# Performance work log

Measured on AMD Instinct MI355X. Metric: run time of the kernel, lower is better.

Reference implementation:

```python
import jax, jax.numpy as jnp
import numpy as np

N_NODES = 100000
N_EDGES = 1200000
K1, K2 = 4096, 256  # TopKPooling ratios (int ratio => absolute k in PyG)
NEG_SLOPE = 0.01    # nn.LeakyReLU default


def leaky(v):
    return jnp.where(v >= 0, v, NEG_SLOPE * v)


def gcn_conv(x, src, dst, w, W, b):
    """PyG GCNConv: x @ W, symmetric-normalized aggregation with self-loops, + bias.
    Removed edges are represented by weight 0 (identical math to edge removal)."""
    N = x.shape[0]
    x = x @ W                                            # [N, out]
    deg = jax.ops.segment_sum(w, dst, num_segments=N) + 1.0  # +1 self-loop
    dinv = jax.lax.rsqrt(deg)
    norm = dinv[src] * w * dinv[dst]                     # per-edge norm
    agg = jax.ops.segment_sum(x[src] * norm[:, None], dst, num_segments=N)
    agg = agg + x * (dinv * dinv)[:, None]               # self-loop term
    return agg + b


def topk_pool(x, src, dst, w, p, k):
    """PyG TopKPooling: score = tanh(x.p/||p||), keep top-k, scale by score,
    relabel edges; dropped edges get weight 0 (mapped to node 0 harmlessly)."""
    N = x.shape[0]
    score = jnp.tanh((x @ p) / jnp.linalg.norm(p))
    top_scores, perm = jax.lax.top_k(score, k)
    x_new = x[perm] * top_scores[:, None]
    mapping = jnp.zeros(N, jnp.int32).at[perm].set(jnp.arange(k, dtype=jnp.int32))
    kept = jnp.zeros(N, dtype=bool).at[perm].set(True)
    valid = kept[src] & kept[dst]
    return x_new, mapping[src], mapping[dst], jnp.where(valid, w, 0.0)


def setup_inputs() -> dict:
    key = jax.random.key(0)
    ks = jax.random.split(key, 12)
    pos = jax.random.normal(ks[0], (N_NODES, 3), dtype=jnp.float32)
    edge_index = jax.random.randint(ks[1], (2, N_EDGES), 0, N_NODES, dtype=jnp.int64)

    def glorot(k, shape):
        lim = np.sqrt(6.0 / (shape[0] + shape[-1]))
        return jax.random.uniform(k, shape, jnp.float32, -lim, lim)

    return {
        "pos": pos,
        "edge_index": edge_index,
        "W1": glorot(ks[2], (3, 64)),    "b1": jnp.zeros((64,), jnp.float32),
        "W2": glorot(ks[3], (64, 128)),  "b2": jnp.zeros((128,), jnp.float32),
        "W3": glorot(ks[4], (128, 256)), "b3": jnp.zeros((256,), jnp.float32),
        "p1": jax.random.normal(ks[5], (64,), jnp.float32),
        "p2": jax.random.normal(ks[6], (256,), jnp.float32),
        "fcW": glorot(ks[7], (256 * 256, 512)),
        "fcb": jnp.zeros((512,), jnp.float32),
    }


def reference(pos, edge_index, W1, b1, W2, b2, W3, b3, p1, p2, fcW, fcb):
    src, dst = edge_index[0], edge_index[1]
    w = jnp.ones(src.shape[0], dtype=pos.dtype)

    x = leaky(gcn_conv(pos, src, dst, w, W1, b1))          # [N, 64]
    x, src, dst, w = topk_pool(x, src, dst, w, p1, K1)     # [4096, 64]
    x = leaky(gcn_conv(x, src, dst, w, W2, b2))            # [4096, 128]
    x = leaky(gcn_conv(x, src, dst, w, W3, b3))            # [4096, 256]
    x, src, dst, w = topk_pool(x, src, dst, w, p2, K2)     # [256, 256]

    x = x.T.reshape(-1)                                    # transpose(0,1) + flatten
    return x @ fcW + fcb                                   # [512]
```

## Files before the change

kernel.cpp:

```cpp
#include <hip/hip_runtime.h>
#include <cstdint>
#include <cstddef>

#define NNODES 100000
#define NEDGES 1200000
#define KP1 4096
#define KP2 256
#define CAP_CAND 16384
#define CAP1 48
#define CAP2 48
#define NSAMP 2048
#define TAURANK 167
#define NXCD 8
#define DRANGE 12500

typedef unsigned long long u64;
typedef unsigned int u32;

__device__ __forceinline__ double leakyd(double v){ return v >= 0.0 ? v : 0.01*v; }

__device__ __forceinline__ u64 mono64(double d){
  u64 b = (u64)__double_as_longlong(d);
  return (b & 0x8000000000000000ull) ? ~b : (b | 0x8000000000000000ull);
}

__device__ __forceinline__ void get_edge(const int* eb, int flag, int e, int& s, int& d){
  if (flag){ s = eb[2*e]; d = eb[2*(NEDGES+e)]; }
  else     { s = eb[e];   d = eb[NEDGES+e]; }
}

__global__ __launch_bounds__(256) void k_zero(int* cnt1, int* mapping, int* rank1, int* rank2, int* cnt){
  int n = blockIdx.x*256 + threadIdx.x;
  if (n < NNODES){ cnt1[n] = 0; mapping[n] = -1; }
  if (n < CAP_CAND) rank1[n] = 0;
  if (n < KP1) rank2[n] = 0;
  if (n < 64) cnt[n] = 0;
}

__global__ void k_meta(const int* eb, const float* p1, const float* p2, int* meta, double* dscal){
  __shared__ double red[256];
  int t = threadIdx.x;
  double s1 = 0.0;
  if (t < 64){ double v = (double)p1[t]; s1 = v*v; }
  red[t] = s1; __syncthreads();
  for (int w = 128; w > 0; w >>= 1){ if (t < w) red[t] += red[t+w]; __syncthreads(); }
  if (t == 0) dscal[0] = 1.0 / sqrt(red[0]);
  __syncthreads();
  double v2 = (double)p2[t];
  red[t] = v2*v2; __syncthreads();
  for (int w = 128; w > 0; w >>= 1){ if (t < w) red[t] += red[t+w]; __syncthreads(); }
  if (t == 0){
    dscal[1] = 1.0 / sqrt(red[0]);
    int is64 = 1;
    for (int i = 1; i <= 127; i += 2) if (eb[i] != 0){ is64 = 0; break; }
    meta[0] = is64;
  }
}

__global__ __launch_bounds__(256) void k_scatter(const int* eb, const int* meta, int* cnt1, int* csrf){
  int e = (blockIdx.x >> 3)*256 + threadIdx.x;
  int x = blockIdx.x & 7;
  if (e >= NEDGES) return;
  int s, d; get_edge(eb, meta[0], e, s, d);
  if (d/DRANGE != x) return;
  int slot = atomicAdd(&cnt1[d], 1);
  if (slot < CAP1) csrf[(size_t)d*CAP1 + slot] = s;
}

__global__ void k_prep(const int* cnt1, const float* pos, double4* posw){
  int n = blockIdx.x*256 + threadIdx.x;
  if (n >= NNODES) return;
  double di = 1.0 / sqrt((double)cnt1[n] + 1.0);
  double4 v;
  v.x = (double)pos[3*n+0]*di;
  v.y = (double)pos[3*n+1]*di;
  v.z = (double)pos[3*n+2]*di;
  v.w = di;
  posw[n] = v;
}

__global__ __launch_bounds__(256) void k_score1(const int* cnt1, const int* csrf,
                         const double4* posw,
                         const float* W1, const float* b1, const float* p1,
                         double* score1raw, u64* key1){
  int gid = blockIdx.x*256 + threadIdx.x;
  int n = gid >> 2;
  int l = gid & 3;
  if (n >= NNODES) return;
  int c = cnt1[n]; if (c > CAP1) c = CAP1;
  const int4* row = (const int4*)(csrf + (size_t)n*CAP1);
  int4 r0 = row[l];
  int4 r1 = make_int4(0,0,0,0);
  int4 r2 = make_int4(0,0,0,0);
  if (c > 16) r1 = row[l+4];
  if (c > 32) r2 = row[l+8];
  double t0 = 0.0, t1 = 0.0, t2 = 0.0;
  auto g = [&](int sidx, bool liv){
    if (liv){
      double4 p = posw[sidx];
      t0 += p.x; t1 += p.y; t2 += p.z;
    }
  };
  int j0 = l*4;
  g(r0.x, j0+0 < c); g(r0.y, j0+1 < c); g(r0.z, j0+2 < c); g(r0.w, j0+3 < c);
  int j1 = l*4 + 16;
  g(r1.x, j1+0 < c); g(r1.y, j1+1 < c); g(r1.z, j1+2 < c); g(r1.w, j1+3 < c);
  int j2 = l*4 + 32;
  g(r2.x, j2+0 < c); g(r2.y, j2+1 < c); g(r2.z, j2+2 < c); g(r2.w, j2+3 < c);
  for (int o = 1; o < 4; o <<= 1){
    t0 += __shfl_xor(t0, o, 64);
    t1 += __shfl_xor(t1, o, 64);
    t2 += __shfl_xor(t2, o, 64);
  }
  double4 pwn = posw[n];
  double di = pwn.w;
  t0 = (t0 + pwn.x)*di;
  t1 = (t1 + pwn.y)*di;
  t2 = (t2 + pwn.z)*di;
  double acc = 0.0;
  #pragma unroll
  for (int f16 = 0; f16 < 16; ++f16){
    int f = l*16 + f16;
    double h = t0*(double)W1[f] + t1*(double)W1[64+f] + t2*(double)W1[128+f] + (double)b1[f];
    acc += leakyd(h) * (double)p1[f];
  }
  acc += __shfl_xor(acc, 1, 64);
  acc += __shfl_xor(acc, 2, 64);
  if (l == 0){
    score1raw[n] = acc;
    key1[n] = (mono64(acc) & ~0x1FFFFull) | (u64)(131071 - n);
  }
}

__global__ __launch_bounds__(256) void k_tau(const u64* key1, u64* tau){
  __shared__ u64 smp[NSAMP];
  int t = threadIdx.x;
  int sid = blockIdx.x*256 + t;
  for (int i = t; i < NSAMP; i += 256) smp[i] = key1[(size_t)i*48];
  __syncthreads();
  u64 mykey = smp[sid];
  int rank = 0;
  for (int j = 0; j < NSAMP; ++j) rank += (smp[j] > mykey) ? 1 : 0;
  if (rank == TAURANK) tau[0] = mykey;
}

__global__ void k_collect(const u64* key1, const u64* tau, int* cand, u64* candkey, int* cnt){
  int n = blockIdx.x*256 + threadIdx.x;
  if (n >= NNODES) return;
  u64 k = key1[n];
  if (k >= tau[0]){
    int p = atomicAdd(&cnt[0], 1);
    if (p < CAP_CAND){ cand[p] = n; candkey[p] = k; }
  }
}

__global__ __launch_bounds__(256) void k_rankA(const u64* candkey, const int* cnt, int* rank){
  int C = cnt[0]; if (C > CAP_CAND) C = CAP_CAND;
  int ci = blockIdx.x, kj = blockIdx.y;
  if (ci*256 >= C || kj*256 >= C) return;
  __shared__ u64 tile[256];
  int t = threadIdx.x;
  int kidx = kj*256 + t;
  tile[t] = (kidx < C) ? candkey[kidx] : 0ull;
  __syncthreads();
  int idx = ci*256 + t;
  if (idx >= C) return;
  u64 mykey = candkey[idx];
  int r = 0;
  #pragma unroll 8
  for (int j = 0; j < 256; ++j) r += (tile[j] > mykey) ? 1 : 0;
  if (r) atomicAdd(&rank[idx], r);
}

__global__ void k_rankB(const int* cand, const int* cnt, const int* rank,
                        int* perm1, int* mapping){
  int idx = blockIdx.x*256 + threadIdx.x;
  int C = cnt[0]; if (C > CAP_CAND) C = CAP_CAND;
  if (idx >= C) return;
  int r = rank[idx];
  if (r < KP1){
    int node = cand[idx];
    perm1[r] = node;
    mapping[node] = r;
  }
}

__global__ __launch_bounds__(256) void k_pool1(const int* perm1, const int* cnt1, const int* csrf,
                          const int* mapping, const double4* posw, const double* score1raw,
                          const float* W1, const float* b1, const double* dscal,
                          int* csr2, int* deg2, double* dinv2, double* x1p){
  int r = blockIdx.x*4 + (threadIdx.x >> 6);
  int l = threadIdx.x & 63;
  int n = perm1[r];
  int c = cnt1[n]; if (c > CAP1) c = CAP1;
  int srcn = -1;
  if (l < c) srcn = csrf[(size_t)n*CAP1 + l];
  int m = -1;
  if (srcn >= 0) m = mapping[srcn];
  u64 bal = __ballot(m >= 0);
  int pre = __popcll(bal & ((1ull << l) - 1ull));
  if (m >= 0 && pre < CAP2) csr2[r*CAP2 + pre] = m;
  if (l == 0){
    int k = __popcll(bal); if (k > CAP2) k = CAP2;
    deg2[r] = k;
    dinv2[r] = 1.0 / sqrt((double)k + 1.0);
  }
  double t0 = 0.0, t1 = 0.0, t2 = 0.0;
  if (l < c){
    double4 p = posw[srcn];
    t0 = p.x; t1 = p.y; t2 = p.z;
  }
  #pragma unroll
  for (int o = 1; o < 64; o <<= 1){
    t0 += __shfl_xor(t0, o, 64);
    t1 += __shfl_xor(t1, o, 64);
    t2 += __shfl_xor(t2, o, 64);
  }
  double4 pwn = posw[n];
  double di = pwn.w;
  t0 = (t0 + pwn.x)*di;
  t1 = (t1 + pwn.y)*di;
  t2 = (t2 + pwn.z)*di;
  double sc = tanh(score1raw[n] * dscal[0]);
  double h = t0*(double)W1[l] + t1*(double)W1[64+l] + t2*(double)W1[128+l] + (double)b1[l];
  x1p[r*64+l] = leakyd(h) * sc;
}

__global__ __launch_bounds__(128) void k_x2(const int* csr2, const int* deg2, const double* dinv2,
                                            const double* x1p, const float* W2, const float* b2, double* x2){
  __shared__ double xin[64];
  int r = blockIdx.x, t = threadIdx.x;
  double dr = dinv2[r];
  if (t < 64){
    double a = 0.0;
    int c = deg2[r];
    for (int j = 0; j < c; ++j){
      int s = csr2[r*CAP2+j];
      a += x1p[s*64+t]*dinv2[s];
    }
    xin[t] = a*dr + x1p[r*64+t]*dr*dr;
  }
  __syncthreads();
  double acc = 0.0;
  for (int c = 0; c < 64; ++c) acc += xin[c]*(double)W2[c*128+t];
  x2[r*128+t] = leakyd(acc + (double)b2[t]);
}

__global__ __launch_bounds__(256) void k_x3(const int* csr2, const int* deg2, const double* dinv2,
                                            const double* x2, const float* W3, const float* b3,
                                            const float* p2, const double* dscal,
                                            double* x3, double* score2, u64* key2){
  __shared__ double xin[128];
  __shared__ double red[256];
  int r = blockIdx.x, t = threadIdx.x;
  double dr = dinv2[r];
  if (t < 128){
    double a = 0.0;
    int c = deg2[r];
    for (int j = 0; j < c; ++j){
      int s = csr2[r*CAP2+j];
      a += x2[s*128+t]*dinv2[s];
    }
    xin[t] = a*dr + x2[r*128+t]*dr*dr;
  }
  __syncthreads();
  double acc = 0.0;
  for (int c = 0; c < 128; ++c) acc += xin[c]*(double)W3[c*256+t];
  double val = leakyd(acc + (double)b3[t]);
  x3[r*256+t] = val;
  red[t] = val * (double)p2[t];
  __syncthreads();
  for (int w = 128; w > 0; w >>= 1){ if (t < w) red[t] += red[t+w]; __syncthreads(); }
  if (t == 0){
    score2[r] = tanh(red[0] * dscal[1]);
    key2[r] = (mono64(red[0]) & ~0x1FFFFull) | (u64)(131071 - r);
  }
}

__global__ __launch_bounds__(256) void k_rank2A(const u64* key2, int* rank2){
  __shared__ u64 tile[256];
  int t = threadIdx.x;
  tile[t] = key2[blockIdx.y*256 + t];
  __syncthreads();
  int idx = blockIdx.x*256 + t;
  u64 mykey = key2[idx];
  int r = 0;
  #pragma unroll 8
  for (int j = 0; j < 256; ++j) r += (tile[j] > mykey) ? 1 : 0;
  if (r) atomicAdd(&rank2[idx], r);
}

__global__ void k_rank2B(const int* rank2, const double* score2, int* perm2, double* sc2){
  int idx = blockIdx.x*256 + threadIdx.x;
  int r = rank2[idx];
  if (r < KP2){
    perm2[r] = idx;
    sc2[r] = score2[idx];
  }
}

__global__ __launch_bounds__(512) void k_fc(const double* x3, const int* perm2, const double* sc2,
                                            const float* fcW, double* partial){
  __shared__ double xs[128];
  int b = blockIdx.x, t = threadIdx.x;
  if (t < 128){
    int f = b >> 1;
    int n = ((b & 1) << 7) + t;
    xs[t] = x3[(size_t)perm2[n]*256 + f] * sc2[n];
  }
  __syncthreads();
  const float* Wp = fcW + (size_t)b*128*512 + t;
  double acc = 0.0;
  #pragma unroll 8
  for (int i = 0; i < 128; ++i) acc += xs[i]*(double)Wp[(size_t)i*512];
  partial[b*512+t] = acc;
}

__global__ __launch_bounds__(128) void k_out(const double* partial, const float* fcb, float* out){
  __shared__ double red[128];
  int o = blockIdx.x, t = threadIdx.x;
  double a = 0.0;
  for (int b = t; b < 512; b += 128) a += partial[(size_t)b*512+o];
  red[t] = a; __syncthreads();
  for (int w = 64; w > 0; w >>= 1){ if (t < w) red[t] += red[t+w]; __syncthreads(); }
  if (t == 0) out[o] = (float)(red[0] + (double)fcb[o]);
}

extern "C" void kernel_launch(void* const* d_in, const int* in_sizes, int n_in,
                              void* d_out, int out_size, void* d_ws, size_t ws_size,
                              hipStream_t stream){
  const float* pos = (const float*)d_in[0];
  const int*   eb  = (const int*)d_in[1];
  const float* W1  = (const float*)d_in[2];
  const float* b1  = (const float*)d_in[3];
  const float* W2  = (const float*)d_in[4];
  const float* b2  = (const float*)d_in[5];
  const float* W3  = (const float*)d_in[6];
  const float* b3  = (const float*)d_in[7];
  const float* p1  = (const float*)d_in[8];
  const float* p2  = (const float*)d_in[9];
  const float* fcW = (const float*)d_in[10];
  const float* fcb = (const float*)d_in[11];
  float* out = (float*)d_out;

  char* w = (char*)d_ws;
  size_t off = 0;
  auto alloc = [&](size_t bytes)->char*{
    char* p = w + off; off = (off + bytes + 255) & ~(size_t)255; return p;
  };
  int*   cnt1   = (int*)  alloc((size_t)NNODES*4);
  int*   cnt    = (int*)  alloc(64*4);
  int*   rank1  = (int*)  alloc(CAP_CAND*4);
  int*   rank2  = (int*)  alloc(KP1*4);
  int*   mapping= (int*)  alloc((size_t)NNODES*4);
  int*    meta  = (int*)  alloc(64*4);
  double* dscal = (double*)alloc(8*8);
  u64*   tau    = (u64*)  alloc(8*8);
  double4* posw = (double4*)alloc((size_t)NNODES*32);
  double* score1= (double*)alloc((size_t)NNODES*8);
  u64*   key1   = (u64*)  alloc((size_t)NNODES*8);
  int*   cand   = (int*)  alloc(CAP_CAND*4);
  u64*   candkey= (u64*)  alloc(CAP_CAND*8);
  int*   perm1  = (int*)  alloc(KP1*4);
  double* x1p   = (double*)alloc((size_t)KP1*64*8);
  int*   csr2   = (int*)  alloc((size_t)KP1*CAP2*4);
  int*   deg2   = (int*)  alloc(KP1*4);
  double* dinv2 = (double*)alloc(KP1*8);
  char*  csrf_base = alloc((size_t)NNODES*CAP1*4);
  int*   csrf   = (int*)csrf_base;
  size_t aoff = 0;
  auto alloc2 = [&](size_t bytes)->char*{
    char* p = csrf_base + aoff; aoff = (aoff + bytes + 255) & ~(size_t)255; return p;
  };
  double* x2    = (double*)alloc2((size_t)KP1*128*8);
  double* x3    = (double*)alloc2((size_t)KP1*256*8);
  double* score2= (double*)alloc2(KP1*8);
  u64*   key2   = (u64*)  alloc2(KP1*8);
  int*   perm2  = (int*)  alloc2(KP2*4);
  double* sc2   = (double*)alloc2(KP2*8);
  double* partial=(double*)alloc2((size_t)512*512*8);
  if (off > ws_size) return;

  k_zero<<<(NNODES+255)/256,256,0,stream>>>(cnt1, mapping, rank1, rank2, cnt);
  k_meta<<<1,256,0,stream>>>(eb, p1, p2, meta, dscal);
  k_scatter<<<((NEDGES+255)/256)*NXCD,256,0,stream>>>(eb, meta, cnt1, csrf);
  k_prep<<<(NNODES+255)/256,256,0,stream>>>(cnt1, pos, posw);
  k_score1<<<(NNODES*4+255)/256,256,0,stream>>>(cnt1, csrf, posw, W1, b1, p1,
                                                score1, key1);
  k_tau<<<NSAMP/256,256,0,stream>>>(key1, tau);
  k_collect<<<(NNODES+255)/256,256,0,stream>>>(key1, tau, cand, candkey, cnt);
  {
    dim3 g(CAP_CAND/256, CAP_CAND/256);
    k_rankA<<<g,256,0,stream>>>(candkey, cnt, rank1);
  }
  k_rankB<<<CAP_CAND/256,256,0,stream>>>(cand, cnt, rank1, perm1, mapping);
  k_pool1<<<KP1/4,256,0,stream>>>(perm1, cnt1, csrf, mapping, posw, score1, W1, b1, dscal,
                                  csr2, deg2, dinv2, x1p);
  k_x2<<<KP1,128,0,stream>>>(csr2, deg2, dinv2, x1p, W2, b2, x2);
  k_x3<<<KP1,256,0,stream>>>(csr2, deg2, dinv2, x2, W3, b3, p2, dscal, x3, score2, key2);
  {
    dim3 g(KP1/256, KP1/256);
    k_rank2A<<<g,256,0,stream>>>(key2, rank2);
  }
  k_rank2B<<<KP1/256,256,0,stream>>>(rank2, score2, perm2, sc2);
  k_fc<<<512,512,0,stream>>>(x3, perm2, sc2, fcW, partial);
  k_out<<<512,128,0,stream>>>(partial, fcb, out);
}
```

Before: 216.5 us.

## Merge init kernels, widen score1 lanes per node, vectorize fc weight loads

Folds the norm/meta computation into the zeroing kernel so one launch replaces two. k_score1 now uses 16 lanes per node instead of 4, giving each lane one neighbor gather per 16-slot chunk and 4 output features, with deeper shuffle reductions. k_fc uses 128 threads per block that each load float4 weight vectors and accumulate four outputs, which cuts thread count and widens memory transactions. The wider score1 mapping launches 4x more threads and adds shuffle overhead in exchange for more memory-level parallelism.

```diff
diff --git a/kernel.cpp b/kernel.cpp
--- a/kernel.cpp
+++ b/kernel.cpp
@@ -29,31 +29,32 @@
   else     { s = eb[e];   d = eb[NEDGES+e]; }
 }
 
-__global__ __launch_bounds__(256) void k_zero(int* cnt1, int* mapping, int* rank1, int* rank2, int* cnt){
+__global__ __launch_bounds__(256) void k_init(const int* eb, const float* p1, const float* p2,
+                       int* meta, double* dscal,
+                       int* cnt1, int* mapping, int* rank1, int* rank2, int* cnt){
   int n = blockIdx.x*256 + threadIdx.x;
   if (n < NNODES){ cnt1[n] = 0; mapping[n] = -1; }
   if (n < CAP_CAND) rank1[n] = 0;
   if (n < KP1) rank2[n] = 0;
   if (n < 64) cnt[n] = 0;
-}
-
-__global__ void k_meta(const int* eb, const float* p1, const float* p2, int* meta, double* dscal){
-  __shared__ double red[256];
-  int t = threadIdx.x;
-  double s1 = 0.0;
-  if (t < 64){ double v = (double)p1[t]; s1 = v*v; }
-  red[t] = s1; __syncthreads();
-  for (int w = 128; w > 0; w >>= 1){ if (t < w) red[t] += red[t+w]; __syncthreads(); }
-  if (t == 0) dscal[0] = 1.0 / sqrt(red[0]);
-  __syncthreads();
-  double v2 = (double)p2[t];
-  red[t] = v2*v2; __syncthreads();
-  for (int w = 128; w > 0; w >>= 1){ if (t < w) red[t] += red[t+w]; __syncthreads(); }
-  if (t == 0){
-    dscal[1] = 1.0 / sqrt(red[0]);
-    int is64 = 1;
-    for (int i = 1; i <= 127; i += 2) if (eb[i] != 0){ is64 = 0; break; }
-    meta[0] = is64;
+  if (blockIdx.x == 0){
+    __shared__ double red[256];
+    int t = threadIdx.x;
+    double s1 = 0.0;
+    if (t < 64){ double v = (double)p1[t]; s1 = v*v; }
+    red[t] = s1; __syncthreads();
+    for (int w = 128; w > 0; w >>= 1){ if (t < w) red[t] += red[t+w]; __syncthreads(); }
+    if (t == 0) dscal[0] = 1.0 / sqrt(red[0]);
+    __syncthreads();
+    double v2 = (double)p2[t];
+    red[t] = v2*v2; __syncthreads();
+    for (int w = 128; w > 0; w >>= 1){ if (t < w) red[t] += red[t+w]; __syncthreads(); }
+    if (t == 0){
+      dscal[1] = 1.0 / sqrt(red[0]);
+      int is64 = 1;
+      for (int i = 1; i <= 127; i += 2) if (eb[i] != 0){ is64 = 0; break; }
+      meta[0] = is64;
+    }
   }
 }
 
@@ -84,30 +85,20 @@
                          const float* W1, const float* b1, const float* p1,
                          double* score1raw, u64* key1){
   int gid = blockIdx.x*256 + threadIdx.x;
-  int n = gid >> 2;
-  int l = gid & 3;
+  int n = gid >> 4;
+  int l = gid & 15;
   if (n >= NNODES) return;
   int c = cnt1[n]; if (c > CAP1) c = CAP1;
-  const int4* row = (const int4*)(csrf + (size_t)n*CAP1);
-  int4 r0 = row[l];
-  int4 r1 = make_int4(0,0,0,0);
-  int4 r2 = make_int4(0,0,0,0);
-  if (c > 16) r1 = row[l+4];
-  if (c > 32) r2 = row[l+8];
+  const int* row = csrf + (size_t)n*CAP1;
+  int r0 = row[l];
+  int r1 = (c > 16) ? row[l+16] : 0;
+  int r2 = (c > 32) ? row[l+32] : 0;
   double t0 = 0.0, t1 = 0.0, t2 = 0.0;
-  auto g = [&](int sidx, bool liv){
-    if (liv){
-      double4 p = posw[sidx];
-      t0 += p.x; t1 += p.y; t2 += p.z;
-    }
-  };
-  int j0 = l*4;
-  g(r0.x, j0+0 < c); g(r0.y, j0+1 < c); g(r0.z, j0+2 < c); g(r0.w, j0+3 < c);
-  int j1 = l*4 + 16;
-  g(r1.x, j1+0 < c); g(r1.y, j1+1 < c); g(r1.z, j1+2 < c); g(r1.w, j1+3 < c);
-  int j2 = l*4 + 32;
-  g(r2.x, j2+0 < c); g(r2.y, j2+1 < c); g(r2.z, j2+2 < c); g(r2.w, j2+3 < c);
-  for (int o = 1; o < 4; o <<= 1){
+  if (l < c){      double4 p = posw[r0]; t0 += p.x; t1 += p.y; t2 += p.z; }
+  if (l+16 < c){   double4 p = posw[r1]; t0 += p.x; t1 += p.y; t2 += p.z; }
+  if (l+32 < c){   double4 p = posw[r2]; t0 += p.x; t1 += p.y; t2 += p.z; }
+  #pragma unroll
+  for (int o = 1; o < 16; o <<= 1){
     t0 += __shfl_xor(t0, o, 64);
     t1 += __shfl_xor(t1, o, 64);
     t2 += __shfl_xor(t2, o, 64);
@@ -119,13 +110,13 @@
   t2 = (t2 + pwn.z)*di;
   double acc = 0.0;
   #pragma unroll
-  for (int f16 = 0; f16 < 16; ++f16){
-    int f = l*16 + f16;
+  for (int f4 = 0; f4 < 4; ++f4){
+    int f = l*4 + f4;
     double h = t0*(double)W1[f] + t1*(double)W1[64+f] + t2*(double)W1[128+f] + (double)b1[f];
     acc += leakyd(h) * (double)p1[f];
   }
-  acc += __shfl_xor(acc, 1, 64);
-  acc += __shfl_xor(acc, 2, 64);
+  #pragma unroll
+  for (int o = 1; o < 16; o <<= 1) acc += __shfl_xor(acc, o, 64);
   if (l == 0){
     score1raw[n] = acc;
     key1[n] = (mono64(acc) & ~0x1FFFFull) | (u64)(131071 - n);
@@ -299,21 +290,27 @@
   }
 }
 
-__global__ __launch_bounds__(512) void k_fc(const double* x3, const int* perm2, const double* sc2,
+__global__ __launch_bounds__(128) void k_fc(const double* x3, const int* perm2, const double* sc2,
                                             const float* fcW, double* partial){
   __shared__ double xs[128];
   int b = blockIdx.x, t = threadIdx.x;
-  if (t < 128){
+  {
     int f = b >> 1;
     int n = ((b & 1) << 7) + t;
     xs[t] = x3[(size_t)perm2[n]*256 + f] * sc2[n];
   }
   __syncthreads();
-  const float* Wp = fcW + (size_t)b*128*512 + t;
-  double acc = 0.0;
-  #pragma unroll 8
-  for (int i = 0; i < 128; ++i) acc += xs[i]*(double)Wp[(size_t)i*512];
-  partial[b*512+t] = acc;
+  const float4* Wp = (const float4*)(fcW + (size_t)b*128*512) + t;
+  double a0 = 0.0, a1 = 0.0, a2 = 0.0, a3 = 0.0;
+  #pragma unroll 4
+  for (int i = 0; i < 128; ++i){
+    float4 wv = Wp[(size_t)i*128];
+    double xv = xs[i];
+    a0 += xv*(double)wv.x; a1 += xv*(double)wv.y;
+    a2 += xv*(double)wv.z; a3 += xv*(double)wv.w;
+  }
+  double* po = partial + (size_t)b*512 + 4*t;
+  po[0] = a0; po[1] = a1; po[2] = a2; po[3] = a3;
 }
 
 __global__ __launch_bounds__(128) void k_out(const double* partial, const float* fcb, float* out){
@@ -381,12 +378,12 @@
   double* partial=(double*)alloc2((size_t)512*512*8);
   if (off > ws_size) return;
 
-  k_zero<<<(NNODES+255)/256,256,0,stream>>>(cnt1, mapping, rank1, rank2, cnt);
-  k_meta<<<1,256,0,stream>>>(eb, p1, p2, meta, dscal);
+  k_init<<<(NNODES+255)/256,256,0,stream>>>(eb, p1, p2, meta, dscal,
+                                            cnt1, mapping, rank1, rank2, cnt);
   k_scatter<<<((NEDGES+255)/256)*NXCD,256,0,stream>>>(eb, meta, cnt1, csrf);
   k_prep<<<(NNODES+255)/256,256,0,stream>>>(cnt1, pos, posw);
-  k_score1<<<(NNODES*4+255)/256,256,0,stream>>>(cnt1, csrf, posw, W1, b1, p1,
-                                                score1, key1);
+  k_score1<<<(NNODES*16+255)/256,256,0,stream>>>(cnt1, csrf, posw, W1, b1, p1,
+                                                 score1, key1);
   k_tau<<<NSAMP/256,256,0,stream>>>(key1, tau);
   k_collect<<<(NNODES+255)/256,256,0,stream>>>(key1, tau, cand, candkey, cnt);
   {
@@ -403,6 +400,6 @@
     k_rank2A<<<g,256,0,stream>>>(key2, rank2);
   }
   k_rank2B<<<KP1/256,256,0,stream>>>(rank2, score2, perm2, sc2);
-  k_fc<<<512,512,0,stream>>>(x3, perm2, sc2, fcW, partial);
+  k_fc<<<512,128,0,stream>>>(x3, perm2, sc2, fcW, partial);
   k_out<<<512,128,0,stream>>>(partial, fcb, out);
 }
```

Measured after the change: 208.1 us (median of 2 runs). 1.04x faster.
